# Optimization experiments

Hardware: AMD Instinct MI355X
Metric: run time of the kernel (lower is better)

The kernel has to match this reference:

```python
import jax, jax.numpy as jnp
import numpy as np

B = 4             # graphs per batch
POS_RANGE = 240.0 # pos lives in [0, 240)^3
VOXELS = (20.0, 30.0, 50.0, 80.0)
NEG = -1e30


def _basis(u):
    # open B-spline basis, degree 1, kernel_size 2, dim 3 -> 8 weights per edge
    cols = []
    for k in range(8):
        w = (u[:, 0] if k & 4 else 1.0 - u[:, 0])
        w = w * (u[:, 1] if k & 2 else 1.0 - u[:, 1])
        w = w * (u[:, 2] if k & 1 else 1.0 - u[:, 2])
        cols.append(w)
    return jnp.stack(cols, axis=1)  # [E, 8]


def _cartesian(pos, src, dst, emask):
    # T.Cartesian(cat=False, norm=True): rel pos scaled into [0,1]
    rel = pos[src] - pos[dst]
    m = jnp.max(jnp.where(emask[:, None], jnp.abs(rel), 0.0))
    return rel / (2.0 * jnp.maximum(m, 1e-9)) + 0.5


def _spline_conv(x, src, dst, pseudo, emask, W, Wr, b, n_nodes):
    # out_i = mean_{j->i} sum_k B_k(u_ij) x_j W_k + x_i Wr + b
    basis = _basis(pseudo) * emask[:, None].astype(x.dtype)  # [E,8]
    xk = jnp.einsum('ni,kio->nko', x, W)                     # [N,8,O]
    msg = basis[:, 0, None] * xk[src, 0]
    for k in range(1, 8):
        msg = msg + basis[:, k, None] * xk[src, k]           # [E,O]
    agg = jax.ops.segment_sum(msg, dst, num_segments=n_nodes)
    deg = jax.ops.segment_sum(emask.astype(x.dtype), dst, num_segments=n_nodes)
    return agg / jnp.maximum(deg, 1.0)[:, None] + x @ Wr + b


def _voxel_ids(pos, batch, vs):
    G = int(np.ceil(POS_RANGE / vs))
    c = jnp.clip(jnp.floor(pos / vs).astype(jnp.int64), 0, G - 1)
    cell = (c[:, 0] * G + c[:, 1]) * G + c[:, 2]
    return batch * (G ** 3) + cell, G ** 3


def _max_pool(x, pos, batch, valid, src, dst, emask, vs):
    # voxel-grid max pooling: nodes become fixed voxel cells (empty cells masked)
    nid, ncells = _voxel_ids(pos, batch, vs)
    n_new = B * ncells
    xm = jnp.where(valid[:, None], x, NEG)
    x_p = jax.ops.segment_max(xm, nid, num_segments=n_new)
    cnt = jax.ops.segment_sum(valid.astype(x.dtype), nid, num_segments=n_new)
    v_new = cnt > 0
    x_p = jnp.where(v_new[:, None], x_p, 0.0)
    pos_p = jax.ops.segment_sum(pos * valid[:, None].astype(pos.dtype), nid, num_segments=n_new)
    pos_p = pos_p / jnp.maximum(cnt, 1.0)[:, None]
    batch_p = jnp.arange(n_new, dtype=jnp.int64) // ncells
    # coarsen edges: remap to cells, drop self loops, coalesce at fixed size
    s2, d2 = nid[src], nid[dst]
    sent = n_new * n_new
    key = jnp.where(emask & (s2 != d2), s2 * n_new + d2, sent)
    uk = jnp.unique(key, size=key.shape[0], fill_value=sent)
    em = uk != sent
    uk = jnp.where(em, uk, 0)
    return x_p, pos_p, batch_p, v_new, uk // n_new, uk % n_new, em


def setup_inputs():
    key = jax.random.key(0)
    ks = jax.random.split(key, 24)
    NP, DEG = 5000, 8
    N = B * NP
    E = N * DEG
    x = jax.random.normal(ks[0], (N, 1), dtype=jnp.float32)
    pos = jax.random.uniform(ks[1], (N, 3), dtype=jnp.float32) * POS_RANGE
    src = jnp.repeat(jnp.arange(N, dtype=jnp.int64), DEG)
    delta = jax.random.randint(ks[2], (E,), 1, 100, dtype=jnp.int64)
    dst = (src // NP) * NP + (src % NP + delta) % NP   # intra-graph edges
    edge_index = jnp.stack([src, dst])
    batch = jnp.arange(N, dtype=jnp.int64) // NP
    sizes = [1, 64, 128, 256, 512]
    params = {}
    for l in range(4):
        ci, co = sizes[l], sizes[l + 1]
        params[f'W{l+1}'] = jax.random.normal(ks[3 + 3 * l], (8, ci, co), dtype=jnp.float32) / np.sqrt(8.0 * ci)
        params[f'Wr{l+1}'] = jax.random.normal(ks[4 + 3 * l], (ci, co), dtype=jnp.float32) / np.sqrt(float(ci))
        params[f'b{l+1}'] = jnp.zeros((co,), dtype=jnp.float32)
    params['fc1_w'] = jax.random.normal(ks[16], (64 * 512, 1024), dtype=jnp.float32) / np.sqrt(64.0 * 512.0)
    params['fc1_b'] = jnp.zeros((1024,), dtype=jnp.float32)
    params['fc2_w'] = jax.random.normal(ks[17], (1024, 1), dtype=jnp.float32) / np.sqrt(1024.0)
    params['fc2_b'] = jnp.zeros((1,), dtype=jnp.float32)
    return dict(x=x, pos=pos, edge_index=edge_index, batch=batch, **params)


def reference(x, pos, edge_index, batch, W1, Wr1, b1, W2, Wr2, b2, W3, Wr3, b3,
              W4, Wr4, b4, fc1_w, fc1_b, fc2_w, fc2_b):
    src, dst = edge_index[0], edge_index[1]
    n_nodes = x.shape[0]
    valid = jnp.ones((n_nodes,), dtype=bool)
    emask = jnp.ones((src.shape[0],), dtype=bool)
    Ws = [(W1, Wr1, b1), (W2, Wr2, b2), (W3, Wr3, b3), (W4, Wr4, b4)]
    for l in range(4):
        pseudo = _cartesian(pos, src, dst, emask)
        W, Wr, b = Ws[l]
        x = jax.nn.elu(_spline_conv(x, src, dst, pseudo, emask, W, Wr, b, n_nodes))
        if l < 3:
            x, pos, batch, valid, src, dst, emask = _max_pool(x, pos, batch, valid, src, dst, emask, VOXELS[l])
            n_nodes = x.shape[0]
    # MaxPoolingX(voxel=80, size=64): ceil(240/80)^3 = 27 <= 64 slots per graph
    nid, ncells = _voxel_ids(pos, batch, VOXELS[3])
    cluster = batch * 64 + (nid % ncells)
    xm = jnp.where(valid[:, None], x, NEG)
    xg = jax.ops.segment_max(xm, cluster, num_segments=B * 64)
    xg = jnp.where(xg <= NEG / 2, 0.0, xg)      # empty slots -> 0 (scatter-max default)
    xg = xg.reshape(B, 64 * 512)
    h = jax.nn.elu(xg @ fc1_w + fc1_b)           # dropout = identity (eval mode)
    return jax.nn.elu(h @ fc2_w + fc2_b)         # [B, 1]
```

## Files before the change

### kernel.cpp

```cpp
#include <hip/hip_runtime.h>

static constexpr int E0 = 160000;
static constexpr int NL0 = 20000;
static constexpr int NL1 = 6912;
static constexpr int NL2 = 2048;
static constexpr int NL3 = 500;

typedef short bf16x8 __attribute__((ext_vector_type(8)));
typedef float f32x4 __attribute__((ext_vector_type(4)));

__device__ __forceinline__ unsigned f2ord(float f) {
  unsigned u = __float_as_uint(f);
  return (u & 0x80000000u) ? ~u : (u | 0x80000000u);
}
__device__ __forceinline__ float ord2f(unsigned u) {
  unsigned v = (u & 0x80000000u) ? (u & 0x7fffffffu) : ~u;
  return __uint_as_float(v);
}
__device__ __forceinline__ float eluf(float x) { return x > 0.f ? x : expm1f(x); }
__device__ __forceinline__ void basis8(float u0, float u1, float u2, float* w) {
  float a0 = 1.f - u0, a1 = 1.f - u1, a2 = 1.f - u2;
  w[0] = a0*a1*a2; w[1] = a0*a1*u2; w[2] = a0*u1*a2; w[3] = a0*u1*u2;
  w[4] = u0*a1*a2; w[5] = u0*a1*u2; w[6] = u0*u1*a2; w[7] = u0*u1*u2;
}
__device__ __forceinline__ unsigned short f2b(float f) {
  unsigned u = __float_as_uint(f);
  return (unsigned short)((u + 0x7fffu + ((u >> 16) & 1u)) >> 16);
}
__device__ __forceinline__ float b2f(unsigned short h) {
  return __uint_as_float(((unsigned)h) << 16);
}
__device__ __forceinline__ int clampi(int v, int lo, int hi) {
  return v < lo ? lo : (v > hi ? hi : v);
}

__global__ void k_deg_absmax(const int* __restrict__ src, const int* __restrict__ dst,
                             const float* __restrict__ pos, int n,
                             int* __restrict__ degi, float* __restrict__ m) {
  float v = 0.f;
  for (int e = blockIdx.x * blockDim.x + threadIdx.x; e < n;
       e += gridDim.x * blockDim.x) {
    int s = src[e], d = dst[e];
    atomicAdd(&degi[d], 1);
    #pragma unroll
    for (int c = 0; c < 3; c++)
      v = fmaxf(v, fabsf(pos[s*3+c] - pos[d*3+c]));
  }
  for (int off = 32; off; off >>= 1) v = fmaxf(v, __shfl_down(v, off, 64));
  __shared__ float red[4];
  int lane = threadIdx.x & 63, wv = threadIdx.x >> 6;
  if (lane == 0) red[wv] = v;
  __syncthreads();
  if (threadIdx.x == 0) {
    float mm = fmaxf(fmaxf(red[0], red[1]), fmaxf(red[2], red[3]));
    atomicMax((unsigned*)m, __float_as_uint(mm));
  }
}

__global__ __launch_bounds__(256)
void k_wprep(const float* __restrict__ W1, const float* __restrict__ Wr1, float* __restrict__ wc1,
             const float* __restrict__ W2, const float* __restrict__ Wr2,
             const float* __restrict__ W3, const float* __restrict__ Wr3,
             const float* __restrict__ W4, const float* __restrict__ Wr4,
             unsigned short* __restrict__ w2h, unsigned short* __restrict__ w2l,
             unsigned short* __restrict__ w3h, unsigned short* __restrict__ w3l,
             unsigned short* __restrict__ w4h, unsigned short* __restrict__ w4l) {
  __shared__ float T[64][65];
  int b = blockIdx.x;
  const float *W, *Wr; unsigned short *oh, *ol; int K, N, kt, nt;
  if (b < 18)      { W = W2; Wr = Wr2; oh = w2h; ol = w2l; K = 576;  N = 128; kt = b / 2;        nt = b % 2; }
  else if (b < 90) { int q = b - 18; W = W3; Wr = Wr3; oh = w3h; ol = w3l; K = 1152; N = 256; kt = q / 4; nt = q % 4; }
  else             { int q = b - 90; W = W4; Wr = Wr4; oh = w4h; ol = w4l; K = 2304; N = 512; kt = q / 8; nt = q % 8; }
  int k0 = kt * 64, n0 = nt * 64, KW = K - K / 9;
  for (int i = threadIdx.x; i < 4096; i += 256) {
    int kk = i >> 6, nn = i & 63; int k = k0 + kk;
    T[kk][nn] = (k < KW) ? W[(long)k * N + n0 + nn] : Wr[(long)(k - KW) * N + n0 + nn];
  }
  __syncthreads();
  for (int i = threadIdx.x; i < 4096; i += 256) {
    int nn = i >> 6, kk = i & 63;
    float v = T[kk][nn];
    unsigned short hu = f2b(v);
    unsigned short lu = f2b(v - b2f(hu));
    long o = (long)(n0 + nn) * K + k0 + kk;
    oh[o] = hu; ol[o] = lu;
  }
  if (b == 0)
    for (int i = threadIdx.x; i < 576; i += 256)
      wc1[i] = (i < 512) ? W1[i] : Wr1[i - 512];
}

__global__ __launch_bounds__(1024)
void k_scan(int* __restrict__ degi, int* __restrict__ rowptr,
            int* __restrict__ cursor, int N) {
  __shared__ int wsum[16];
  __shared__ int woff[16];
  __shared__ int sbase, stot;
  int lane = threadIdx.x & 63, wv = threadIdx.x >> 6;
  if (threadIdx.x == 0) sbase = 0;
  __syncthreads();
  for (int c0 = 0; c0 < N; c0 += 1024) {
    int i = c0 + threadIdx.x;
    int v = (i < N) ? degi[i] : 0;
    int s = v;
    #pragma unroll
    for (int off = 1; off < 64; off <<= 1) {
      int t = __shfl_up(s, off, 64);
      if (lane >= off) s += t;
    }
    if (lane == 63) wsum[wv] = s;
    __syncthreads();
    if (threadIdx.x < 64) {
      int tv = (lane < 16) ? wsum[lane] : 0;
      int ss = tv;
      #pragma unroll
      for (int off = 1; off < 16; off <<= 1) {
        int t = __shfl_up(ss, off, 64);
        if (lane >= off) ss += t;
      }
      if (lane < 16) woff[lane] = ss - tv;
      if (lane == 15) stot = ss;
    }
    __syncthreads();
    int excl = sbase + woff[wv] + s - v;
    if (i < N) { rowptr[i] = excl; cursor[i] = excl; degi[i] = 0; }
    __syncthreads();
    if (threadIdx.x == 0) sbase += stot;
    __syncthreads();
  }
  if (threadIdx.x == 0) rowptr[N] = sbase;
}

__global__ void k_scatter(const int* __restrict__ src, const int* __restrict__ dst,
                          const int* __restrict__ ecnt, int ecap,
                          int* __restrict__ cursor, int* __restrict__ esrc,
                          unsigned* __restrict__ bm, long bmw) {
  long gs = (long)gridDim.x * blockDim.x;
  for (long i = (long)blockIdx.x * blockDim.x + threadIdx.x; i < bmw; i += gs) bm[i] = 0u;
  int n = ecnt ? *ecnt : ecap;
  for (int e = blockIdx.x * blockDim.x + threadIdx.x; e < n;
       e += gridDim.x * blockDim.x) {
    int p = atomicAdd(&cursor[dst[e]], 1);
    esrc[p] = src[e];
  }
}

__global__ __launch_bounds__(256)
void k_l1fused(const float* __restrict__ pos, const float* __restrict__ x0,
               const int* __restrict__ esrc, const int* __restrict__ rowptr,
               const float* __restrict__ m, const float* __restrict__ wc1,
               const float* __restrict__ b1,
               unsigned* __restrict__ pord, float* __restrict__ cnt,
               float* __restrict__ possum, int* __restrict__ nid) {
  int d = blockIdx.x * 4 + (threadIdx.x >> 6);
  int lane = threadIdx.x & 63;
  if (d >= NL0) return;
  float inv = 0.5f / fmaxf(m[0], 1e-9f);
  float pd0 = pos[d*3], pd1 = pos[d*3+1], pd2 = pos[d*3+2];
  int beg = rowptr[d], end = rowptr[d+1];
  float acc[8] = {};
  for (int j = beg; j < end; j++) {
    int s = esrc[j];
    float u0 = (pos[s*3+0] - pd0) * inv + 0.5f;
    float u1 = (pos[s*3+1] - pd1) * inv + 0.5f;
    float u2 = (pos[s*3+2] - pd2) * inv + 0.5f;
    float w[8]; basis8(u0, u1, u2, w);
    float xv = x0[s];
    #pragma unroll
    for (int k = 0; k < 8; k++) acc[k] += w[k] * xv;
  }
  float sc = 1.f / fmaxf((float)(end - beg), 1.f);
  float v = b1[lane] + x0[d] * wc1[512 + lane];
  #pragma unroll
  for (int k = 0; k < 8; k++) v += acc[k] * sc * wc1[k * 64 + lane];
  v = eluf(v);
  int c0 = clampi((int)floorf(pd0 / 20.f), 0, 11);
  int c1 = clampi((int)floorf(pd1 / 20.f), 0, 11);
  int c2 = clampi((int)floorf(pd2 / 20.f), 0, 11);
  int id = (d / 5000) * 1728 + (c0 * 12 + c1) * 12 + c2;
  atomicMax(&pord[(long)id * 64 + lane], f2ord(v));
  if (lane == 0) {
    nid[d] = id;
    atomicAdd(&cnt[id], 1.f);
    atomicAdd(&possum[id*3+0], pd0);
    atomicAdd(&possum[id*3+1], pd1);
    atomicAdd(&possum[id*3+2], pd2);
  }
}

__global__ __launch_bounds__(256)
void k_gather(const float* __restrict__ pos, const float* __restrict__ x,
              const int* __restrict__ esrc, const int* __restrict__ rowptr,
              const float* __restrict__ m,
              unsigned short* __restrict__ ysh, unsigned short* __restrict__ ysl,
              int N, int Ci, int nchunk,
              unsigned* __restrict__ zptr, long zn) {
  long gs = (long)gridDim.x * blockDim.x;
  for (long i = (long)blockIdx.x * blockDim.x + threadIdx.x; i < zn; i += gs) zptr[i] = 0u;
  int wid = blockIdx.x * 4 + (threadIdx.x >> 6);
  int lane = threadIdx.x & 63;
  int d = wid / nchunk, ch = wid % nchunk;
  if (d >= N) return;
  int co = ch * 64 + lane;
  float inv = 0.5f / fmaxf(m[0], 1e-9f);
  float pd0 = pos[d*3], pd1 = pos[d*3+1], pd2 = pos[d*3+2];
  int beg = rowptr[d], end = rowptr[d+1];
  float acc[8] = {};
  int s_cur = (beg < end) ? esrc[beg] : 0;
  for (int j = beg; j < end; j++) {
    int s = s_cur;
    s_cur = (j + 1 < end) ? esrc[j + 1] : 0;
    float u0 = (pos[s*3+0] - pd0) * inv + 0.5f;
    float u1 = (pos[s*3+1] - pd1) * inv + 0.5f;
    float u2 = (pos[s*3+2] - pd2) * inv + 0.5f;
    float w[8]; basis8(u0, u1, u2, w);
    float xv = x[(long)s * Ci + co];
    #pragma unroll
    for (int k = 0; k < 8; k++) acc[k] += w[k] * xv;
  }
  float sc = 1.f / fmaxf((float)(end - beg), 1.f);
  long row = (long)d * 9 * Ci;
  #pragma unroll
  for (int k = 0; k < 8; k++) {
    float v = acc[k] * sc;
    unsigned short hu = f2b(v);
    ysh[row + k * Ci + co] = hu;
    ysl[row + k * Ci + co] = f2b(v - b2f(hu));
  }
  float xd = x[(long)d * Ci + co];
  unsigned short hu = f2b(xd);
  ysh[row + 8 * Ci + co] = hu;
  ysl[row + 8 * Ci + co] = f2b(xd - b2f(hu));
}

__global__ __launch_bounds__(256)
void k_gemm_mfma(const unsigned short* __restrict__ Ah, const unsigned short* __restrict__ Al,
                 const unsigned short* __restrict__ Bh, const unsigned short* __restrict__ Bl,
                 float* __restrict__ Cp, int M, int N, int K, int ksl, long zstride) {
  __shared__ unsigned short Ash[64][40], Asl[64][40], Bsh[64][40], Bsl[64][40];
  int m0 = blockIdx.y * 64, n0 = blockIdx.x * 64;
  int kbeg = blockIdx.z * ksl;
  int t = threadIdx.x, w = t >> 6, lane = t & 63;
  int r = t >> 2, sg = (t & 3) * 8;
  f32x4 acc[4] = {};
  for (int kt = 0; kt < ksl; kt += 32) {
    bf16x8 va = {}, vb = {};
    if (m0 + r < M) {
      long ga = (long)(m0 + r) * K + kbeg + kt + sg;
      va = *(const bf16x8*)&Ah[ga];
      vb = *(const bf16x8*)&Al[ga];
    }
    *(bf16x8*)&Ash[r][sg] = va;
    *(bf16x8*)&Asl[r][sg] = vb;
    long gb = (long)(n0 + r) * K + kbeg + kt + sg;
    *(bf16x8*)&Bsh[r][sg] = *(const bf16x8*)&Bh[gb];
    *(bf16x8*)&Bsl[r][sg] = *(const bf16x8*)&Bl[gb];
    __syncthreads();
    int ar = (w << 4) + (lane & 15), kq = (lane >> 4) << 3;
    bf16x8 ah = *(const bf16x8*)&Ash[ar][kq];
    bf16x8 al = *(const bf16x8*)&Asl[ar][kq];
    #pragma unroll
    for (int nt = 0; nt < 4; nt++) {
      int br = (nt << 4) + (lane & 15);
      bf16x8 bh = *(const bf16x8*)&Bsh[br][kq];
      bf16x8 bl = *(const bf16x8*)&Bsl[br][kq];
      acc[nt] = __builtin_amdgcn_mfma_f32_16x16x32_bf16(al, bh, acc[nt], 0, 0, 0);
      acc[nt] = __builtin_amdgcn_mfma_f32_16x16x32_bf16(ah, bl, acc[nt], 0, 0, 0);
      acc[nt] = __builtin_amdgcn_mfma_f32_16x16x32_bf16(ah, bh, acc[nt], 0, 0, 0);
    }
    __syncthreads();
  }
  float* Co = Cp + zstride * blockIdx.z;
  int row0 = m0 + (w << 4) + ((lane >> 4) << 2);
  int col = n0 + (lane & 15);
  #pragma unroll
  for (int nt = 0; nt < 4; nt++)
    #pragma unroll
    for (int q = 0; q < 4; q++) {
      int gm = row0 + q;
      if (gm < M) Co[(long)gm * N + col + nt * 16] = acc[nt][q];
    }
}

__global__ void k_reduce_pool(const float* __restrict__ Cp, const float* __restrict__ bias,
                              long MN, int Co, int z,
                              const float* __restrict__ pos, const unsigned char* __restrict__ valid,
                              int div, float vs, int G, int SLOT,
                              unsigned* __restrict__ pord, float* __restrict__ cnt,
                              float* __restrict__ possum, int* __restrict__ nid) {
  long idx = (long)blockIdx.x * blockDim.x + threadIdx.x;
  if (idx >= MN) return;
  int n = (int)(idx / Co), o = (int)(idx % Co);
  float s = 0.f;
  for (int q = 0; q < z; q++) s += Cp[q * MN + idx];
  float v = eluf(s + bias[o]);
  float p0 = pos[n*3], p1 = pos[n*3+1], p2 = pos[n*3+2];
  int c0 = clampi((int)floorf(p0 / vs), 0, G - 1);
  int c1 = clampi((int)floorf(p1 / vs), 0, G - 1);
  int c2 = clampi((int)floorf(p2 / vs), 0, G - 1);
  int id = (n / div) * SLOT + (c0 * G + c1) * G + c2;
  if (o == 0 && nid) nid[n] = id;
  if (!valid[n]) return;
  atomicMax(&pord[(long)id * Co + o], f2ord(v));
  if (o == 0 && cnt) {
    atomicAdd(&cnt[id], 1.f);
    atomicAdd(&possum[id*3+0], p0);
    atomicAdd(&possum[id*3+1], p1);
    atomicAdd(&possum[id*3+2], p2);
  }
}

__global__ void k_pool_fin(const unsigned* __restrict__ pord, const float* __restrict__ cnt,
                           const float* __restrict__ possum, float* __restrict__ xp,
                           float* __restrict__ posp, unsigned char* __restrict__ validp,
                           int Nn, int Cf) {
  long idx = (long)blockIdx.x * blockDim.x + threadIdx.x;
  if (idx >= (long)Nn * Cf) return;
  int n = (int)(idx / Cf), o = (int)(idx % Cf);
  float c = cnt[n];
  xp[idx] = (c > 0.f) ? ord2f(pord[idx]) : 0.f;
  if (o == 0) {
    validp[n] = (c > 0.f) ? 1 : 0;
    float ic = 1.f / fmaxf(c, 1.f);
    posp[n*3+0] = possum[n*3+0] * ic;
    posp[n*3+1] = possum[n*3+1] * ic;
    posp[n*3+2] = possum[n*3+2] * ic;
  }
}

__global__ void k_pool_edges(const int* __restrict__ srcf, const int* __restrict__ dstf,
                             const int* __restrict__ ecntf, int ecap,
                             const int* __restrict__ nid, int Nn,
                             unsigned* __restrict__ bitmap,
                             int* __restrict__ srcc, int* __restrict__ dstc,
                             int* __restrict__ ecntc, int* __restrict__ degi,
                             const float* __restrict__ posp, float* __restrict__ m) {
  int n = ecntf ? *ecntf : ecap;
  float vmax = 0.f;
  for (int e = blockIdx.x * blockDim.x + threadIdx.x; e < n;
       e += gridDim.x * blockDim.x) {
    int s2 = nid[srcf[e]], d2 = nid[dstf[e]];
    if (s2 == d2) continue;
    #pragma unroll
    for (int c = 0; c < 3; c++)
      vmax = fmaxf(vmax, fabsf(posp[s2*3+c] - posp[d2*3+c]));
    unsigned key = (unsigned)s2 * (unsigned)Nn + (unsigned)d2;
    unsigned bit = 1u << (key & 31);
    unsigned old = atomicOr(&bitmap[key >> 5], bit);
    if (!(old & bit)) {
      int p = atomicAdd(ecntc, 1);
      srcc[p] = s2; dstc[p] = d2;
      atomicAdd(&degi[d2], 1);
    }
  }
  for (int off = 32; off; off >>= 1) vmax = fmaxf(vmax, __shfl_down(vmax, off, 64));
  __shared__ float red[4];
  int lane = threadIdx.x & 63, wv = threadIdx.x >> 6;
  if (lane == 0) red[wv] = vmax;
  __syncthreads();
  if (threadIdx.x == 0) {
    float mm = fmaxf(fmaxf(red[0], red[1]), fmaxf(red[2], red[3]));
    atomicMax((unsigned*)m, __float_as_uint(mm));
  }
}

__global__ __launch_bounds__(128)
void k_fc1(const unsigned* __restrict__ xg_ord, const float* __restrict__ w,
           float* __restrict__ h) {
  int cellhalf = blockIdx.x >> 3, jb = blockIdx.x & 7;
  int cell = cellhalf >> 1, half = cellhalf & 1;
  int j = jb * 128 + threadIdx.x;
  __shared__ float xs[4][256];
  for (int q = threadIdx.x; q < 1024; q += 128) {
    int b = q >> 8, ci = q & 255;
    unsigned o = xg_ord[((b * 64 + cell) << 9) + half * 256 + ci];
    xs[b][ci] = (o == 0u) ? 0.f : ord2f(o);
  }
  __syncthreads();
  float a0 = 0, a1 = 0, a2 = 0, a3 = 0;
  int cbase = cell * 512 + half * 256;
  for (int ci = 0; ci < 256; ci++) {
    float ww = w[(long)(cbase + ci) * 1024 + j];
    a0 += xs[0][ci] * ww; a1 += xs[1][ci] * ww;
    a2 += xs[2][ci] * ww; a3 += xs[3][ci] * ww;
  }
  atomicAdd(&h[j], a0);        atomicAdd(&h[1024 + j], a1);
  atomicAdd(&h[2048 + j], a2); atomicAdd(&h[3072 + j], a3);
}

__global__ void k_fc2(const float* __restrict__ h, const float* __restrict__ fb1,
                      const float* __restrict__ w, const float* __restrict__ b,
                      float* __restrict__ out) {
  int bb = blockIdx.x, t = threadIdx.x;
  float a = 0;
  for (int j = t; j < 1024; j += 256) a += eluf(h[bb * 1024 + j] + fb1[j]) * w[j];
  for (int off = 32; off; off >>= 1) a += __shfl_down(a, off, 64);
  __shared__ float red[4];
  int lane = t & 63, wv = t >> 6;
  if (lane == 0) red[wv] = a;
  __syncthreads();
  if (t == 0) out[bb] = eluf(red[0] + red[1] + red[2] + red[3] + b[0]);
}

extern "C" void kernel_launch(void* const* d_in, const int* in_sizes, int n_in,
                              void* d_out, int out_size, void* d_ws, size_t ws_size,
                              hipStream_t stream) {
  const float* x0   = (const float*)d_in[0];
  const float* pos0 = (const float*)d_in[1];
  const int*   ei   = (const int*)d_in[2];
  const float* W1 = (const float*)d_in[4],  *Wr1 = (const float*)d_in[5],  *b1 = (const float*)d_in[6];
  const float* W2 = (const float*)d_in[7],  *Wr2 = (const float*)d_in[8],  *b2 = (const float*)d_in[9];
  const float* W3 = (const float*)d_in[10], *Wr3 = (const float*)d_in[11], *b3 = (const float*)d_in[12];
  const float* W4 = (const float*)d_in[13], *Wr4 = (const float*)d_in[14], *b4 = (const float*)d_in[15];
  const float* fw1 = (const float*)d_in[16], *fb1 = (const float*)d_in[17];
  const float* fw2 = (const float*)d_in[18], *fb2 = (const float*)d_in[19];
  float* out = (float*)d_out;
  const int* src0 = ei;
  const int* dst0 = ei + E0;

  char* ws = (char*)d_ws;
  size_t off = 0;
  auto alloc = [&](size_t bytes) -> void* {
    off = (off + 255) & ~(size_t)255;
    void* p = ws + off; off += bytes; return p;
  };
  int* src1 = (int*)alloc(E0 * 4); int* dst1 = (int*)alloc(E0 * 4);
  int* src2 = (int*)alloc(E0 * 4); int* dst2 = (int*)alloc(E0 * 4);
  int* src3 = (int*)alloc(E0 * 4); int* dst3 = (int*)alloc(E0 * 4);
  float* x1p = (float*)alloc((size_t)NL1 * 64 * 4);
  float* x2p = (float*)alloc((size_t)NL2 * 128 * 4);
  float* x3p = (float*)alloc((size_t)NL3 * 256 * 4);
  float* pos1 = (float*)alloc(NL1 * 12);
  float* pos2 = (float*)alloc(NL2 * 12);
  float* pos3 = (float*)alloc(NL3 * 12);
  unsigned char* val1 = (unsigned char*)alloc(NL1);
  unsigned char* val2 = (unsigned char*)alloc(NL2);
  unsigned char* val3 = (unsigned char*)alloc(NL3);
  unsigned short* ysh = (unsigned short*)alloc((size_t)NL1 * 576 * 2);
  unsigned short* ysl = (unsigned short*)alloc((size_t)NL1 * 576 * 2);
  float* wc1 = (float*)alloc(576 * 4);
  unsigned short* w2h = (unsigned short*)alloc((size_t)576 * 128 * 2);
  unsigned short* w2l = (unsigned short*)alloc((size_t)576 * 128 * 2);
  unsigned short* w3h = (unsigned short*)alloc((size_t)1152 * 256 * 2);
  unsigned short* w3l = (unsigned short*)alloc((size_t)1152 * 256 * 2);
  unsigned short* w4h = (unsigned short*)alloc((size_t)2304 * 512 * 2);
  unsigned short* w4l = (unsigned short*)alloc((size_t)2304 * 512 * 2);
  float* Cp  = (float*)alloc((size_t)6 * 2048 * 256 * 4);
  int* nid    = (int*)alloc(NL0 * 4);
  int* rowptr = (int*)alloc((NL0 + 1) * 4);
  int* cursor = (int*)alloc(NL0 * 4);
  int* esrc   = (int*)alloc(E0 * 4);
  char* zA = (char*)alloc(0);
  float* h      = (float*)alloc(4096 * 4);
  float* cnt    = (float*)alloc(NL1 * 4);
  float* possum = (float*)alloc(NL1 * 12);
  unsigned* pord = (unsigned*)alloc((size_t)NL1 * 64 * 4);
  char* zAend = (char*)alloc(0);
  int* degi = (int*)alloc(NL0 * 4);
  size_t bmwords = ((size_t)NL1 * NL1 + 31) / 32;
  unsigned* bitmap = (unsigned*)alloc(bmwords * 4);
  float* mbuf = (float*)alloc(64);
  int* ecnt = (int*)(mbuf + 8);
  char* zend = (char*)alloc(0);
  long zAn = (long)(zAend - zA) / 4;
  size_t zbytes = (size_t)(zend - zA);
  unsigned* xg_ord = pord + (size_t)NL3 * 256;
  (void)ws_size; (void)in_sizes; (void)n_in; (void)out_size;

  auto cdiv = [](long a, long b) { return (int)((a + b - 1) / b); };

  hipMemsetAsync(zA, 0, zbytes, stream);

  k_deg_absmax<<<512, 256, 0, stream>>>(src0, dst0, pos0, E0, degi, mbuf + 0);
  k_wprep<<<378, 256, 0, stream>>>(W1, Wr1, wc1, W2, Wr2, W3, Wr3, W4, Wr4,
                                   w2h, w2l, w3h, w3l, w4h, w4l);
  k_scan<<<1, 1024, 0, stream>>>(degi, rowptr, cursor, NL0);
  k_scatter<<<512, 256, 0, stream>>>(src0, dst0, nullptr, E0, cursor, esrc, bitmap, bmwords);

  k_l1fused<<<5000, 256, 0, stream>>>(pos0, x0, esrc, rowptr, mbuf + 0, wc1, b1,
                                      pord, cnt, possum, nid);
  k_pool_fin<<<cdiv((long)NL1 * 64, 256), 256, 0, stream>>>(pord, cnt, possum, x1p, pos1, val1, NL1, 64);
  k_pool_edges<<<512, 256, 0, stream>>>(src0, dst0, nullptr, E0, nid, NL1, bitmap,
                                        src1, dst1, ecnt + 0, degi, pos1, mbuf + 1);
  k_scan<<<1, 1024, 0, stream>>>(degi, rowptr, cursor, NL1);
  k_scatter<<<512, 256, 0, stream>>>(src1, dst1, ecnt + 0, E0, cursor, esrc, bitmap, bmwords);

  k_gather<<<cdiv(NL1, 4), 256, 0, stream>>>(pos1, x1p, esrc, rowptr, mbuf + 1,
                                             ysh, ysl, NL1, 64, 1, (unsigned*)zA, zAn);
  k_gemm_mfma<<<dim3(2, cdiv(NL1, 64), 3), 256, 0, stream>>>(ysh, ysl, w2h, w2l, Cp,
                                                             NL1, 128, 576, 192, (long)NL1 * 128);
  k_reduce_pool<<<cdiv((long)NL1 * 128, 256), 256, 0, stream>>>(
      Cp, b2, (long)NL1 * 128, 128, 3, pos1, val1, 1728, 30.f, 8, 512, pord, cnt, possum, nid);
  k_pool_fin<<<cdiv((long)NL2 * 128, 256), 256, 0, stream>>>(pord, cnt, possum, x2p, pos2, val2, NL2, 128);
  k_pool_edges<<<512, 256, 0, stream>>>(src1, dst1, ecnt + 0, E0, nid, NL2, bitmap,
                                        src2, dst2, ecnt + 1, degi, pos2, mbuf + 2);
  k_scan<<<1, 1024, 0, stream>>>(degi, rowptr, cursor, NL2);
  k_scatter<<<512, 256, 0, stream>>>(src2, dst2, ecnt + 1, E0, cursor, esrc, bitmap, bmwords);

  k_gather<<<cdiv(NL2 * 2, 4), 256, 0, stream>>>(pos2, x2p, esrc, rowptr, mbuf + 2,
                                                 ysh, ysl, NL2, 128, 2, (unsigned*)zA, zAn);
  k_gemm_mfma<<<dim3(4, cdiv(NL2, 64), 6), 256, 0, stream>>>(ysh, ysl, w3h, w3l, Cp,
                                                             NL2, 256, 1152, 192, (long)NL2 * 256);
  k_reduce_pool<<<cdiv((long)NL2 * 256, 256), 256, 0, stream>>>(
      Cp, b3, (long)NL2 * 256, 256, 6, pos2, val2, 512, 50.f, 5, 125, pord, cnt, possum, nid);
  k_pool_fin<<<cdiv((long)NL3 * 256, 256), 256, 0, stream>>>(pord, cnt, possum, x3p, pos3, val3, NL3, 256);
  k_pool_edges<<<512, 256, 0, stream>>>(src2, dst2, ecnt + 1, E0, nid, NL3, bitmap,
                                        src3, dst3, ecnt + 2, degi, pos3, mbuf + 3);
  k_scan<<<1, 1024, 0, stream>>>(degi, rowptr, cursor, NL3);
  k_scatter<<<512, 256, 0, stream>>>(src3, dst3, ecnt + 2, E0, cursor, esrc, bitmap, bmwords);

  k_gather<<<cdiv(NL3 * 4, 4), 256, 0, stream>>>(pos3, x3p, esrc, rowptr, mbuf + 3,
                                                 ysh, ysl, NL3, 256, 4, (unsigned*)zA, zAn);
  k_gemm_mfma<<<dim3(8, cdiv(NL3, 64), 12), 256, 0, stream>>>(ysh, ysl, w4h, w4l, Cp,
                                                              NL3, 512, 2304, 192, (long)NL3 * 512);
  k_reduce_pool<<<cdiv((long)NL3 * 512, 256), 256, 0, stream>>>(
      Cp, b4, (long)NL3 * 512, 512, 12, pos3, val3, 125, 80.f, 3, 64, xg_ord, nullptr, nullptr, nullptr);

  k_fc1<<<27 * 2 * 8, 128, 0, stream>>>(xg_ord, fw1, h);
  k_fc2<<<4, 256, 0, stream>>>(h, fb1, fw2, fb2, out);
}
```

Baseline: 482.3 us.

## Replace CSR build with atomic linked lists and fuse GEMM with pooling

Replaces the degree-count, scan and scatter CSR construction with per-destination linked lists built through atomicExch. This removes the single-block scan kernels and several launches per layer. Pooling finalisation is folded into the consumers: gather reads pooled max, count and position sums directly, and the GEMM for layers 2 and 3 now runs without K-splitting and scatters pooled results itself. Separate per-layer buffers and bitmaps replace the shared ones. The trade-off is that linked-list traversal is a serially dependent pointer chase, and neighbour order is no longer deterministic.

```diff
diff --git a/kernel.cpp b/kernel.cpp
--- a/kernel.cpp
+++ b/kernel.cpp
@@ -34,229 +34,31 @@
   return v < lo ? lo : (v > hi ? hi : v);
 }
 
-__global__ void k_deg_absmax(const int* __restrict__ src, const int* __restrict__ dst,
-                             const float* __restrict__ pos, int n,
-                             int* __restrict__ degi, float* __restrict__ m) {
-  float v = 0.f;
-  for (int e = blockIdx.x * blockDim.x + threadIdx.x; e < n;
-       e += gridDim.x * blockDim.x) {
-    int s = src[e], d = dst[e];
-    atomicAdd(&degi[d], 1);
-    #pragma unroll
-    for (int c = 0; c < 3; c++)
-      v = fmaxf(v, fabsf(pos[s*3+c] - pos[d*3+c]));
-  }
-  for (int off = 32; off; off >>= 1) v = fmaxf(v, __shfl_down(v, off, 64));
-  __shared__ float red[4];
-  int lane = threadIdx.x & 63, wv = threadIdx.x >> 6;
-  if (lane == 0) red[wv] = v;
-  __syncthreads();
-  if (threadIdx.x == 0) {
-    float mm = fmaxf(fmaxf(red[0], red[1]), fmaxf(red[2], red[3]));
-    atomicMax((unsigned*)m, __float_as_uint(mm));
-  }
-}
-
-__global__ __launch_bounds__(256)
-void k_wprep(const float* __restrict__ W1, const float* __restrict__ Wr1, float* __restrict__ wc1,
-             const float* __restrict__ W2, const float* __restrict__ Wr2,
-             const float* __restrict__ W3, const float* __restrict__ Wr3,
-             const float* __restrict__ W4, const float* __restrict__ Wr4,
-             unsigned short* __restrict__ w2h, unsigned short* __restrict__ w2l,
-             unsigned short* __restrict__ w3h, unsigned short* __restrict__ w3l,
-             unsigned short* __restrict__ w4h, unsigned short* __restrict__ w4l) {
-  __shared__ float T[64][65];
-  int b = blockIdx.x;
-  const float *W, *Wr; unsigned short *oh, *ol; int K, N, kt, nt;
-  if (b < 18)      { W = W2; Wr = Wr2; oh = w2h; ol = w2l; K = 576;  N = 128; kt = b / 2;        nt = b % 2; }
-  else if (b < 90) { int q = b - 18; W = W3; Wr = Wr3; oh = w3h; ol = w3l; K = 1152; N = 256; kt = q / 4; nt = q % 4; }
-  else             { int q = b - 90; W = W4; Wr = Wr4; oh = w4h; ol = w4l; K = 2304; N = 512; kt = q / 8; nt = q % 8; }
-  int k0 = kt * 64, n0 = nt * 64, KW = K - K / 9;
-  for (int i = threadIdx.x; i < 4096; i += 256) {
-    int kk = i >> 6, nn = i & 63; int k = k0 + kk;
-    T[kk][nn] = (k < KW) ? W[(long)k * N + n0 + nn] : Wr[(long)(k - KW) * N + n0 + nn];
-  }
-  __syncthreads();
-  for (int i = threadIdx.x; i < 4096; i += 256) {
-    int nn = i >> 6, kk = i & 63;
-    float v = T[kk][nn];
-    unsigned short hu = f2b(v);
-    unsigned short lu = f2b(v - b2f(hu));
-    long o = (long)(n0 + nn) * K + k0 + kk;
-    oh[o] = hu; ol[o] = lu;
-  }
-  if (b == 0)
-    for (int i = threadIdx.x; i < 576; i += 256)
-      wc1[i] = (i < 512) ? W1[i] : Wr1[i - 512];
-}
-
-__global__ __launch_bounds__(1024)
-void k_scan(int* __restrict__ degi, int* __restrict__ rowptr,
-            int* __restrict__ cursor, int N) {
-  __shared__ int wsum[16];
-  __shared__ int woff[16];
-  __shared__ int sbase, stot;
-  int lane = threadIdx.x & 63, wv = threadIdx.x >> 6;
-  if (threadIdx.x == 0) sbase = 0;
-  __syncthreads();
-  for (int c0 = 0; c0 < N; c0 += 1024) {
-    int i = c0 + threadIdx.x;
-    int v = (i < N) ? degi[i] : 0;
-    int s = v;
-    #pragma unroll
-    for (int off = 1; off < 64; off <<= 1) {
-      int t = __shfl_up(s, off, 64);
-      if (lane >= off) s += t;
-    }
-    if (lane == 63) wsum[wv] = s;
-    __syncthreads();
-    if (threadIdx.x < 64) {
-      int tv = (lane < 16) ? wsum[lane] : 0;
-      int ss = tv;
-      #pragma unroll
-      for (int off = 1; off < 16; off <<= 1) {
-        int t = __shfl_up(ss, off, 64);
-        if (lane >= off) ss += t;
-      }
-      if (lane < 16) woff[lane] = ss - tv;
-      if (lane == 15) stot = ss;
-    }
-    __syncthreads();
-    int excl = sbase + woff[wv] + s - v;
-    if (i < N) { rowptr[i] = excl; cursor[i] = excl; degi[i] = 0; }
-    __syncthreads();
-    if (threadIdx.x == 0) sbase += stot;
-    __syncthreads();
-  }
-  if (threadIdx.x == 0) rowptr[N] = sbase;
-}
-
-__global__ void k_scatter(const int* __restrict__ src, const int* __restrict__ dst,
-                          const int* __restrict__ ecnt, int ecap,
-                          int* __restrict__ cursor, int* __restrict__ esrc,
-                          unsigned* __restrict__ bm, long bmw) {
-  long gs = (long)gridDim.x * blockDim.x;
-  for (long i = (long)blockIdx.x * blockDim.x + threadIdx.x; i < bmw; i += gs) bm[i] = 0u;
-  int n = ecnt ? *ecnt : ecap;
-  for (int e = blockIdx.x * blockDim.x + threadIdx.x; e < n;
-       e += gridDim.x * blockDim.x) {
-    int p = atomicAdd(&cursor[dst[e]], 1);
-    esrc[p] = src[e];
-  }
-}
-
-__global__ __launch_bounds__(256)
-void k_l1fused(const float* __restrict__ pos, const float* __restrict__ x0,
-               const int* __restrict__ esrc, const int* __restrict__ rowptr,
-               const float* __restrict__ m, const float* __restrict__ wc1,
-               const float* __restrict__ b1,
-               unsigned* __restrict__ pord, float* __restrict__ cnt,
-               float* __restrict__ possum, int* __restrict__ nid) {
-  int d = blockIdx.x * 4 + (threadIdx.x >> 6);
-  int lane = threadIdx.x & 63;
-  if (d >= NL0) return;
-  float inv = 0.5f / fmaxf(m[0], 1e-9f);
-  float pd0 = pos[d*3], pd1 = pos[d*3+1], pd2 = pos[d*3+2];
-  int beg = rowptr[d], end = rowptr[d+1];
-  float acc[8] = {};
-  for (int j = beg; j < end; j++) {
-    int s = esrc[j];
-    float u0 = (pos[s*3+0] - pd0) * inv + 0.5f;
-    float u1 = (pos[s*3+1] - pd1) * inv + 0.5f;
-    float u2 = (pos[s*3+2] - pd2) * inv + 0.5f;
-    float w[8]; basis8(u0, u1, u2, w);
-    float xv = x0[s];
-    #pragma unroll
-    for (int k = 0; k < 8; k++) acc[k] += w[k] * xv;
-  }
-  float sc = 1.f / fmaxf((float)(end - beg), 1.f);
-  float v = b1[lane] + x0[d] * wc1[512 + lane];
-  #pragma unroll
-  for (int k = 0; k < 8; k++) v += acc[k] * sc * wc1[k * 64 + lane];
-  v = eluf(v);
-  int c0 = clampi((int)floorf(pd0 / 20.f), 0, 11);
-  int c1 = clampi((int)floorf(pd1 / 20.f), 0, 11);
-  int c2 = clampi((int)floorf(pd2 / 20.f), 0, 11);
-  int id = (d / 5000) * 1728 + (c0 * 12 + c1) * 12 + c2;
-  atomicMax(&pord[(long)id * 64 + lane], f2ord(v));
-  if (lane == 0) {
-    nid[d] = id;
-    atomicAdd(&cnt[id], 1.f);
-    atomicAdd(&possum[id*3+0], pd0);
-    atomicAdd(&possum[id*3+1], pd1);
-    atomicAdd(&possum[id*3+2], pd2);
-  }
-}
-
-__global__ __launch_bounds__(256)
-void k_gather(const float* __restrict__ pos, const float* __restrict__ x,
-              const int* __restrict__ esrc, const int* __restrict__ rowptr,
-              const float* __restrict__ m,
-              unsigned short* __restrict__ ysh, unsigned short* __restrict__ ysl,
-              int N, int Ci, int nchunk,
-              unsigned* __restrict__ zptr, long zn) {
-  long gs = (long)gridDim.x * blockDim.x;
-  for (long i = (long)blockIdx.x * blockDim.x + threadIdx.x; i < zn; i += gs) zptr[i] = 0u;
-  int wid = blockIdx.x * 4 + (threadIdx.x >> 6);
-  int lane = threadIdx.x & 63;
-  int d = wid / nchunk, ch = wid % nchunk;
-  if (d >= N) return;
-  int co = ch * 64 + lane;
-  float inv = 0.5f / fmaxf(m[0], 1e-9f);
-  float pd0 = pos[d*3], pd1 = pos[d*3+1], pd2 = pos[d*3+2];
-  int beg = rowptr[d], end = rowptr[d+1];
-  float acc[8] = {};
-  int s_cur = (beg < end) ? esrc[beg] : 0;
-  for (int j = beg; j < end; j++) {
-    int s = s_cur;
-    s_cur = (j + 1 < end) ? esrc[j + 1] : 0;
-    float u0 = (pos[s*3+0] - pd0) * inv + 0.5f;
-    float u1 = (pos[s*3+1] - pd1) * inv + 0.5f;
-    float u2 = (pos[s*3+2] - pd2) * inv + 0.5f;
-    float w[8]; basis8(u0, u1, u2, w);
-    float xv = x[(long)s * Ci + co];
-    #pragma unroll
-    for (int k = 0; k < 8; k++) acc[k] += w[k] * xv;
-  }
-  float sc = 1.f / fmaxf((float)(end - beg), 1.f);
-  long row = (long)d * 9 * Ci;
-  #pragma unroll
-  for (int k = 0; k < 8; k++) {
-    float v = acc[k] * sc;
-    unsigned short hu = f2b(v);
-    ysh[row + k * Ci + co] = hu;
-    ysl[row + k * Ci + co] = f2b(v - b2f(hu));
-  }
-  float xd = x[(long)d * Ci + co];
-  unsigned short hu = f2b(xd);
-  ysh[row + 8 * Ci + co] = hu;
-  ysl[row + 8 * Ci + co] = f2b(xd - b2f(hu));
-}
-
-__global__ __launch_bounds__(256)
-void k_gemm_mfma(const unsigned short* __restrict__ Ah, const unsigned short* __restrict__ Al,
-                 const unsigned short* __restrict__ Bh, const unsigned short* __restrict__ Bl,
-                 float* __restrict__ Cp, int M, int N, int K, int ksl, long zstride) {
-  __shared__ unsigned short Ash[64][40], Asl[64][40], Bsh[64][40], Bsl[64][40];
-  int m0 = blockIdx.y * 64, n0 = blockIdx.x * 64;
-  int kbeg = blockIdx.z * ksl;
-  int t = threadIdx.x, w = t >> 6, lane = t & 63;
+__device__ __forceinline__ void mfma_tile(const unsigned short* __restrict__ Ah,
+    const unsigned short* __restrict__ Al, const unsigned short* __restrict__ Bh,
+    const unsigned short* __restrict__ Bl, int M, long K, int m0, int n0,
+    int kbeg, int ksl, char* smem, f32x4* acc) {
+  auto Ash = (unsigned short (*)[40])(smem);
+  auto Asl = (unsigned short (*)[40])(smem + 5120);
+  auto Bsh = (unsigned short (*)[40])(smem + 10240);
+  auto Bsl = (unsigned short (*)[40])(smem + 15360);
+  int t = threadIdx.x;
   int r = t >> 2, sg = (t & 3) * 8;
-  f32x4 acc[4] = {};
+  int w = t >> 6, lane = t & 63;
+  int ar = (w << 4) + (lane & 15), kq = (lane >> 4) << 3;
   for (int kt = 0; kt < ksl; kt += 32) {
-    bf16x8 va = {}, vb = {};
+    bf16x8 va = {}, vl = {};
     if (m0 + r < M) {
       long ga = (long)(m0 + r) * K + kbeg + kt + sg;
       va = *(const bf16x8*)&Ah[ga];
-      vb = *(const bf16x8*)&Al[ga];
+      vl = *(const bf16x8*)&Al[ga];
     }
     *(bf16x8*)&Ash[r][sg] = va;
-    *(bf16x8*)&Asl[r][sg] = vb;
+    *(bf16x8*)&Asl[r][sg] = vl;
     long gb = (long)(n0 + r) * K + kbeg + kt + sg;
     *(bf16x8*)&Bsh[r][sg] = *(const bf16x8*)&Bh[gb];
     *(bf16x8*)&Bsl[r][sg] = *(const bf16x8*)&Bl[gb];
     __syncthreads();
-    int ar = (w << 4) + (lane & 15), kq = (lane >> 4) << 3;
     bf16x8 ah = *(const bf16x8*)&Ash[ar][kq];
     bf16x8 al = *(const bf16x8*)&Asl[ar][kq];
     #pragma unroll
@@ -270,98 +72,276 @@
     }
     __syncthreads();
   }
-  float* Co = Cp + zstride * blockIdx.z;
+}
+
+__global__ __launch_bounds__(256)
+void k_prep(const int* __restrict__ src0, const int* __restrict__ dst0,
+            const float* __restrict__ pos0, int* __restrict__ head0,
+            int* __restrict__ next0, float* __restrict__ mbuf,
+            const float* __restrict__ W1, const float* __restrict__ Wr1, float* __restrict__ wc1,
+            const float* __restrict__ W2, const float* __restrict__ Wr2,
+            const float* __restrict__ W3, const float* __restrict__ Wr3,
+            const float* __restrict__ W4, const float* __restrict__ Wr4,
+            unsigned short* __restrict__ w2h, unsigned short* __restrict__ w2l,
+            unsigned short* __restrict__ w3h, unsigned short* __restrict__ w3l,
+            unsigned short* __restrict__ w4h, unsigned short* __restrict__ w4l) {
+  __shared__ __align__(16) float T[64][65];
+  __shared__ float red[4];
+  int tid = blockIdx.x * 256 + threadIdx.x, gsz = gridDim.x * 256;
+  float v = 0.f;
+  for (int e = tid; e < E0; e += gsz) {
+    int s = src0[e], d = dst0[e];
+    next0[e] = atomicExch(&head0[d], e + 1);
+    v = fmaxf(v, fabsf(pos0[s*3]   - pos0[d*3]));
+    v = fmaxf(v, fabsf(pos0[s*3+1] - pos0[d*3+1]));
+    v = fmaxf(v, fabsf(pos0[s*3+2] - pos0[d*3+2]));
+  }
+  #pragma unroll
+  for (int off = 32; off; off >>= 1) v = fmaxf(v, __shfl_down(v, off, 64));
+  if ((threadIdx.x & 63) == 0) red[threadIdx.x >> 6] = v;
+  __syncthreads();
+  if (threadIdx.x == 0)
+    atomicMax((unsigned*)mbuf,
+              __float_as_uint(fmaxf(fmaxf(red[0], red[1]), fmaxf(red[2], red[3]))));
+  for (int b = blockIdx.x; b < 378; b += gridDim.x) {
+    const float *W, *Wr; unsigned short *oh, *ol; int K, N, kt, nt;
+    if (b < 18)      { W = W2; Wr = Wr2; oh = w2h; ol = w2l; K = 576;  N = 128; kt = b / 2; nt = b % 2; }
+    else if (b < 90) { int q = b - 18; W = W3; Wr = Wr3; oh = w3h; ol = w3l; K = 1152; N = 256; kt = q / 4; nt = q % 4; }
+    else             { int q = b - 90; W = W4; Wr = Wr4; oh = w4h; ol = w4l; K = 2304; N = 512; kt = q / 8; nt = q % 8; }
+    int k0 = kt * 64, n0 = nt * 64, KW = K - K / 9;
+    __syncthreads();
+    for (int i = threadIdx.x; i < 4096; i += 256) {
+      int kk = i >> 6, nn = i & 63, k = k0 + kk;
+      T[kk][nn] = (k < KW) ? W[(long)k * N + n0 + nn] : Wr[(long)(k - KW) * N + n0 + nn];
+    }
+    __syncthreads();
+    for (int i = threadIdx.x; i < 4096; i += 256) {
+      int nn = i >> 6, kk = i & 63;
+      float vv = T[kk][nn];
+      unsigned short hu = f2b(vv), lu = f2b(vv - b2f(hu));
+      long o = (long)(n0 + nn) * K + k0 + kk;
+      oh[o] = hu; ol[o] = lu;
+    }
+  }
+  if (blockIdx.x == 0)
+    for (int i = threadIdx.x; i < 576; i += 256)
+      wc1[i] = (i < 512) ? W1[i] : Wr1[i - 512];
+}
+
+__global__ __launch_bounds__(256)
+void k_l1(const float* __restrict__ pos0, const float* __restrict__ x0,
+          const int* __restrict__ src0, const int* __restrict__ head0,
+          const int* __restrict__ next0, const float* __restrict__ mbuf,
+          const float* __restrict__ wc1, const float* __restrict__ b1,
+          unsigned* __restrict__ pord1, float* __restrict__ cnt1,
+          float* __restrict__ possum1, int* __restrict__ nid) {
+  int d = blockIdx.x * 4 + (threadIdx.x >> 6);
+  int lane = threadIdx.x & 63;
+  if (d >= NL0) return;
+  float inv = 0.5f / fmaxf(mbuf[0], 1e-9f);
+  float pd0 = pos0[d*3], pd1 = pos0[d*3+1], pd2 = pos0[d*3+2];
+  float acc[8] = {};
+  int len = 0;
+  for (int j = head0[d]; j; ) {
+    int e = j - 1; j = next0[e];
+    int s = src0[e];
+    float u0 = (pos0[s*3]   - pd0) * inv + 0.5f;
+    float u1 = (pos0[s*3+1] - pd1) * inv + 0.5f;
+    float u2 = (pos0[s*3+2] - pd2) * inv + 0.5f;
+    float w[8]; basis8(u0, u1, u2, w);
+    float xv = x0[s];
+    #pragma unroll
+    for (int k = 0; k < 8; k++) acc[k] += w[k] * xv;
+    len++;
+  }
+  float sc = 1.f / fmaxf((float)len, 1.f);
+  float v = b1[lane] + x0[d] * wc1[512 + lane];
+  #pragma unroll
+  for (int k = 0; k < 8; k++) v += acc[k] * sc * wc1[k * 64 + lane];
+  v = eluf(v);
+  int c0 = clampi((int)floorf(pd0 / 20.f), 0, 11);
+  int c1 = clampi((int)floorf(pd1 / 20.f), 0, 11);
+  int c2 = clampi((int)floorf(pd2 / 20.f), 0, 11);
+  int id = (d / 5000) * 1728 + (c0 * 12 + c1) * 12 + c2;
+  atomicMax(&pord1[(long)id * 64 + lane], f2ord(v));
+  if (lane == 0) {
+    nid[d] = id;
+    atomicAdd(&cnt1[id], 1.f);
+    atomicAdd(&possum1[id*3],   pd0);
+    atomicAdd(&possum1[id*3+1], pd1);
+    atomicAdd(&possum1[id*3+2], pd2);
+  }
+}
+
+__global__ __launch_bounds__(256)
+void k_pedge(const int* __restrict__ srcf, const int* __restrict__ dstf,
+             const int* __restrict__ ecntf, int ecap,
+             const int* __restrict__ nid, int Nn, unsigned* __restrict__ bitmap,
+             int* __restrict__ srcc, int* __restrict__ dstc, int* __restrict__ nextc,
+             int* __restrict__ headc, int* __restrict__ ecntc,
+             const float* __restrict__ possum, const float* __restrict__ cnt,
+             float* __restrict__ mo) {
+  __shared__ float red[4];
+  int n = ecntf ? *ecntf : ecap;
+  float vmax = 0.f;
+  for (int e = blockIdx.x * 256 + threadIdx.x; e < n; e += gridDim.x * 256) {
+    int s2 = nid[srcf[e]], d2 = nid[dstf[e]];
+    if (s2 == d2) continue;
+    float ics = 1.f / fmaxf(cnt[s2], 1.f), icd = 1.f / fmaxf(cnt[d2], 1.f);
+    vmax = fmaxf(vmax, fabsf(possum[s2*3]   * ics - possum[d2*3]   * icd));
+    vmax = fmaxf(vmax, fabsf(possum[s2*3+1] * ics - possum[d2*3+1] * icd));
+    vmax = fmaxf(vmax, fabsf(possum[s2*3+2] * ics - possum[d2*3+2] * icd));
+    unsigned key = (unsigned)s2 * (unsigned)Nn + (unsigned)d2;
+    unsigned bit = 1u << (key & 31);
+    unsigned old = atomicOr(&bitmap[key >> 5], bit);
+    if (!(old & bit)) {
+      int q = atomicAdd(ecntc, 1);
+      srcc[q] = s2; dstc[q] = d2;
+      nextc[q] = atomicExch(&headc[d2], q + 1);
+    }
+  }
+  #pragma unroll
+  for (int off = 32; off; off >>= 1) vmax = fmaxf(vmax, __shfl_down(vmax, off, 64));
+  if ((threadIdx.x & 63) == 0) red[threadIdx.x >> 6] = vmax;
+  __syncthreads();
+  if (threadIdx.x == 0)
+    atomicMax((unsigned*)mo,
+              __float_as_uint(fmaxf(fmaxf(red[0], red[1]), fmaxf(red[2], red[3]))));
+}
+
+__global__ __launch_bounds__(256)
+void k_gather(const float* __restrict__ possum, const float* __restrict__ cnt,
+              const unsigned* __restrict__ pordc,
+              const int* __restrict__ srcarr, const int* __restrict__ head,
+              const int* __restrict__ nextl, const float* __restrict__ mbuf,
+              unsigned short* __restrict__ ysh, unsigned short* __restrict__ ysl,
+              int N, int Ci, int nchunk) {
+  int wid = blockIdx.x * 4 + (threadIdx.x >> 6);
+  int lane = threadIdx.x & 63;
+  int d = wid / nchunk, ch = wid % nchunk;
+  if (d >= N) return;
+  int co = ch * 64 + lane;
+  float inv = 0.5f / fmaxf(mbuf[0], 1e-9f);
+  float cd = cnt[d];
+  float icd = 1.f / fmaxf(cd, 1.f);
+  float pd0 = possum[d*3] * icd, pd1 = possum[d*3+1] * icd, pd2 = possum[d*3+2] * icd;
+  float acc[8] = {};
+  int len = 0;
+  for (int j = head[d]; j; ) {
+    int e = j - 1; j = nextl[e];
+    int s = srcarr[e];
+    float ics = 1.f / fmaxf(cnt[s], 1.f);
+    float u0 = (possum[s*3]   * ics - pd0) * inv + 0.5f;
+    float u1 = (possum[s*3+1] * ics - pd1) * inv + 0.5f;
+    float u2 = (possum[s*3+2] * ics - pd2) * inv + 0.5f;
+    float w[8]; basis8(u0, u1, u2, w);
+    float xv = ord2f(pordc[(long)s * Ci + co]);
+    #pragma unroll
+    for (int k = 0; k < 8; k++) acc[k] += w[k] * xv;
+    len++;
+  }
+  float sc = 1.f / fmaxf((float)len, 1.f);
+  long row = (long)d * 9 * Ci;
+  #pragma unroll
+  for (int k = 0; k < 8; k++) {
+    float v = acc[k] * sc;
+    unsigned short hu = f2b(v);
+    ysh[row + k * Ci + co] = hu;
+    ysl[row + k * Ci + co] = f2b(v - b2f(hu));
+  }
+  float xd = (cd > 0.f) ? ord2f(pordc[(long)d * Ci + co]) : 0.f;
+  unsigned short hu = f2b(xd);
+  ysh[row + 8 * Ci + co] = hu;
+  ysl[row + 8 * Ci + co] = f2b(xd - b2f(hu));
+}
+
+__global__ __launch_bounds__(256)
+void k_gemmpool(const unsigned short* __restrict__ ysh, const unsigned short* __restrict__ ysl,
+                const unsigned short* __restrict__ Bh, const unsigned short* __restrict__ Bl,
+                int M, int N, int K, const float* __restrict__ bias,
+                const float* __restrict__ possum, const float* __restrict__ cnt,
+                int div, float vs, int G, int NC,
+                unsigned* __restrict__ pordn, float* __restrict__ cntn,
+                float* __restrict__ possumn, int* __restrict__ nid) {
+  __shared__ __align__(16) char smem[20480];
+  int nbx = N >> 6;
+  int bx = blockIdx.x % nbx, by = blockIdx.x / nbx;
+  int m0 = by * 64, n0 = bx * 64;
+  f32x4 acc[4] = {};
+  mfma_tile(ysh, ysl, Bh, Bl, M, K, m0, n0, 0, K, smem, acc);
+  int w = threadIdx.x >> 6, lane = threadIdx.x & 63;
   int row0 = m0 + (w << 4) + ((lane >> 4) << 2);
-  int col = n0 + (lane & 15);
+  int colb = n0 + (lane & 15);
+  #pragma unroll
+  for (int q = 0; q < 4; q++) {
+    int gm = row0 + q;
+    float c = cnt[gm];
+    float ic = 1.f / fmaxf(c, 1.f);
+    float p0 = possum[gm*3] * ic, p1 = possum[gm*3+1] * ic, p2 = possum[gm*3+2] * ic;
+    int c0 = clampi((int)floorf(p0 / vs), 0, G - 1);
+    int c1 = clampi((int)floorf(p1 / vs), 0, G - 1);
+    int c2 = clampi((int)floorf(p2 / vs), 0, G - 1);
+    int id = (gm / div) * NC + (c0 * G + c1) * G + c2;
+    bool vl = c > 0.f;
+    if (bx == 0 && (lane & 15) == 0) {
+      nid[gm] = id;
+      if (vl) {
+        atomicAdd(&cntn[id], 1.f);
+        atomicAdd(&possumn[id*3],   p0);
+        atomicAdd(&possumn[id*3+1], p1);
+        atomicAdd(&possumn[id*3+2], p2);
+      }
+    }
+    if (vl) {
+      #pragma unroll
+      for (int nt = 0; nt < 4; nt++) {
+        int col = colb + nt * 16;
+        float v = eluf(acc[nt][q] + bias[col]);
+        atomicMax(&pordn[(long)id * N + col], f2ord(v));
+      }
+    }
+  }
+}
+
+__global__ __launch_bounds__(256)
+void k_gemm4(const unsigned short* __restrict__ ysh, const unsigned short* __restrict__ ysl,
+             const unsigned short* __restrict__ Bh, const unsigned short* __restrict__ Bl,
+             float* __restrict__ Cp) {
+  __shared__ __align__(16) char smem[20480];
+  int z = blockIdx.x >> 6, rem = blockIdx.x & 63, bx = rem & 7, by = rem >> 3;
+  int m0 = by * 64, n0 = bx * 64;
+  f32x4 acc[4] = {};
+  mfma_tile(ysh, ysl, Bh, Bl, 500, 2304, m0, n0, z * 576, 576, smem, acc);
+  float* Co = Cp + (long)z * 256000;
+  int w = threadIdx.x >> 6, lane = threadIdx.x & 63;
+  int row0 = m0 + (w << 4) + ((lane >> 4) << 2);
+  int colb = n0 + (lane & 15);
   #pragma unroll
   for (int nt = 0; nt < 4; nt++)
     #pragma unroll
     for (int q = 0; q < 4; q++) {
       int gm = row0 + q;
-      if (gm < M) Co[(long)gm * N + col + nt * 16] = acc[nt][q];
-    }
-}
-
-__global__ void k_reduce_pool(const float* __restrict__ Cp, const float* __restrict__ bias,
-                              long MN, int Co, int z,
-                              const float* __restrict__ pos, const unsigned char* __restrict__ valid,
-                              int div, float vs, int G, int SLOT,
-                              unsigned* __restrict__ pord, float* __restrict__ cnt,
-                              float* __restrict__ possum, int* __restrict__ nid) {
-  long idx = (long)blockIdx.x * blockDim.x + threadIdx.x;
-  if (idx >= MN) return;
-  int n = (int)(idx / Co), o = (int)(idx % Co);
-  float s = 0.f;
-  for (int q = 0; q < z; q++) s += Cp[q * MN + idx];
-  float v = eluf(s + bias[o]);
-  float p0 = pos[n*3], p1 = pos[n*3+1], p2 = pos[n*3+2];
-  int c0 = clampi((int)floorf(p0 / vs), 0, G - 1);
-  int c1 = clampi((int)floorf(p1 / vs), 0, G - 1);
-  int c2 = clampi((int)floorf(p2 / vs), 0, G - 1);
-  int id = (n / div) * SLOT + (c0 * G + c1) * G + c2;
-  if (o == 0 && nid) nid[n] = id;
-  if (!valid[n]) return;
-  atomicMax(&pord[(long)id * Co + o], f2ord(v));
-  if (o == 0 && cnt) {
-    atomicAdd(&cnt[id], 1.f);
-    atomicAdd(&possum[id*3+0], p0);
-    atomicAdd(&possum[id*3+1], p1);
-    atomicAdd(&possum[id*3+2], p2);
-  }
-}
-
-__global__ void k_pool_fin(const unsigned* __restrict__ pord, const float* __restrict__ cnt,
-                           const float* __restrict__ possum, float* __restrict__ xp,
-                           float* __restrict__ posp, unsigned char* __restrict__ validp,
-                           int Nn, int Cf) {
-  long idx = (long)blockIdx.x * blockDim.x + threadIdx.x;
-  if (idx >= (long)Nn * Cf) return;
-  int n = (int)(idx / Cf), o = (int)(idx % Cf);
-  float c = cnt[n];
-  xp[idx] = (c > 0.f) ? ord2f(pord[idx]) : 0.f;
-  if (o == 0) {
-    validp[n] = (c > 0.f) ? 1 : 0;
-    float ic = 1.f / fmaxf(c, 1.f);
-    posp[n*3+0] = possum[n*3+0] * ic;
-    posp[n*3+1] = possum[n*3+1] * ic;
-    posp[n*3+2] = possum[n*3+2] * ic;
-  }
-}
-
-__global__ void k_pool_edges(const int* __restrict__ srcf, const int* __restrict__ dstf,
-                             const int* __restrict__ ecntf, int ecap,
-                             const int* __restrict__ nid, int Nn,
-                             unsigned* __restrict__ bitmap,
-                             int* __restrict__ srcc, int* __restrict__ dstc,
-                             int* __restrict__ ecntc, int* __restrict__ degi,
-                             const float* __restrict__ posp, float* __restrict__ m) {
-  int n = ecntf ? *ecntf : ecap;
-  float vmax = 0.f;
-  for (int e = blockIdx.x * blockDim.x + threadIdx.x; e < n;
-       e += gridDim.x * blockDim.x) {
-    int s2 = nid[srcf[e]], d2 = nid[dstf[e]];
-    if (s2 == d2) continue;
-    #pragma unroll
-    for (int c = 0; c < 3; c++)
-      vmax = fmaxf(vmax, fabsf(posp[s2*3+c] - posp[d2*3+c]));
-    unsigned key = (unsigned)s2 * (unsigned)Nn + (unsigned)d2;
-    unsigned bit = 1u << (key & 31);
-    unsigned old = atomicOr(&bitmap[key >> 5], bit);
-    if (!(old & bit)) {
-      int p = atomicAdd(ecntc, 1);
-      srcc[p] = s2; dstc[p] = d2;
-      atomicAdd(&degi[d2], 1);
-    }
-  }
-  for (int off = 32; off; off >>= 1) vmax = fmaxf(vmax, __shfl_down(vmax, off, 64));
-  __shared__ float red[4];
-  int lane = threadIdx.x & 63, wv = threadIdx.x >> 6;
-  if (lane == 0) red[wv] = vmax;
-  __syncthreads();
-  if (threadIdx.x == 0) {
-    float mm = fmaxf(fmaxf(red[0], red[1]), fmaxf(red[2], red[3]));
-    atomicMax((unsigned*)m, __float_as_uint(mm));
-  }
+      if (gm < 500) Co[(long)gm * 512 + colb + nt * 16] = acc[nt][q];
+    }
+}
+
+__global__ void k_reduce4(const float* __restrict__ Cp, const float* __restrict__ b4,
+                          const float* __restrict__ possum3, const float* __restrict__ cnt3,
+                          unsigned* __restrict__ xg) {
+  int idx = blockIdx.x * 256 + threadIdx.x;
+  if (idx >= 256000) return;
+  int n = idx >> 9, o = idx & 511;
+  float s = Cp[idx] + Cp[idx + 256000] + Cp[idx + 512000] + Cp[idx + 768000];
+  float v = eluf(s + b4[o]);
+  float c = cnt3[n];
+  if (c <= 0.f) return;
+  float ic = 1.f / c;
+  float p0 = possum3[n*3] * ic, p1 = possum3[n*3+1] * ic, p2 = possum3[n*3+2] * ic;
+  int c0 = clampi((int)floorf(p0 / 80.f), 0, 2);
+  int c1 = clampi((int)floorf(p1 / 80.f), 0, 2);
+  int c2 = clampi((int)floorf(p2 / 80.f), 0, 2);
+  int cl = (n / 125) * 64 + (c0 * 3 + c1) * 3 + c2;
+  atomicMax(&xg[(long)cl * 512 + o], f2ord(v));
 }
 
 __global__ __launch_bounds__(128)
@@ -422,20 +402,13 @@
   size_t off = 0;
   auto alloc = [&](size_t bytes) -> void* {
     off = (off + 255) & ~(size_t)255;
-    void* p = ws + off; off += bytes; return p;
+    void* q = ws + off; off += bytes; return q;
   };
-  int* src1 = (int*)alloc(E0 * 4); int* dst1 = (int*)alloc(E0 * 4);
-  int* src2 = (int*)alloc(E0 * 4); int* dst2 = (int*)alloc(E0 * 4);
-  int* src3 = (int*)alloc(E0 * 4); int* dst3 = (int*)alloc(E0 * 4);
-  float* x1p = (float*)alloc((size_t)NL1 * 64 * 4);
-  float* x2p = (float*)alloc((size_t)NL2 * 128 * 4);
-  float* x3p = (float*)alloc((size_t)NL3 * 256 * 4);
-  float* pos1 = (float*)alloc(NL1 * 12);
-  float* pos2 = (float*)alloc(NL2 * 12);
-  float* pos3 = (float*)alloc(NL3 * 12);
-  unsigned char* val1 = (unsigned char*)alloc(NL1);
-  unsigned char* val2 = (unsigned char*)alloc(NL2);
-  unsigned char* val3 = (unsigned char*)alloc(NL3);
+  int* next0 = (int*)alloc(E0 * 4);
+  int* src1 = (int*)alloc(E0 * 4); int* dst1 = (int*)alloc(E0 * 4); int* next1 = (int*)alloc(E0 * 4);
+  int* src2 = (int*)alloc(E0 * 4); int* dst2 = (int*)alloc(E0 * 4); int* next2 = (int*)alloc(E0 * 4);
+  int* src3 = (int*)alloc(E0 * 4); int* dst3 = (int*)alloc(E0 * 4); int* next3 = (int*)alloc(E0 * 4);
+  int* nid  = (int*)alloc(NL0 * 4);
   unsigned short* ysh = (unsigned short*)alloc((size_t)NL1 * 576 * 2);
   unsigned short* ysl = (unsigned short*)alloc((size_t)NL1 * 576 * 2);
   float* wc1 = (float*)alloc(576 * 4);
@@ -445,77 +418,67 @@
   unsigned short* w3l = (unsigned short*)alloc((size_t)1152 * 256 * 2);
   unsigned short* w4h = (unsigned short*)alloc((size_t)2304 * 512 * 2);
   unsigned short* w4l = (unsigned short*)alloc((size_t)2304 * 512 * 2);
-  float* Cp  = (float*)alloc((size_t)6 * 2048 * 256 * 4);
-  int* nid    = (int*)alloc(NL0 * 4);
-  int* rowptr = (int*)alloc((NL0 + 1) * 4);
-  int* cursor = (int*)alloc(NL0 * 4);
-  int* esrc   = (int*)alloc(E0 * 4);
-  char* zA = (char*)alloc(0);
-  float* h      = (float*)alloc(4096 * 4);
-  float* cnt    = (float*)alloc(NL1 * 4);
-  float* possum = (float*)alloc(NL1 * 12);
-  unsigned* pord = (unsigned*)alloc((size_t)NL1 * 64 * 4);
-  char* zAend = (char*)alloc(0);
-  int* degi = (int*)alloc(NL0 * 4);
-  size_t bmwords = ((size_t)NL1 * NL1 + 31) / 32;
-  unsigned* bitmap = (unsigned*)alloc(bmwords * 4);
+  float* Cp = (float*)alloc((size_t)4 * 256000 * 4);
+  char* z0 = (char*)alloc(0);
+  int* head0 = (int*)alloc(NL0 * 4);
+  int* head1 = (int*)alloc(NL1 * 4);
+  int* head2 = (int*)alloc(NL2 * 4);
+  int* head3 = (int*)alloc(NL3 * 4);
+  unsigned* pord1 = (unsigned*)alloc((size_t)NL1 * 64 * 4);
+  unsigned* pord2 = (unsigned*)alloc((size_t)NL2 * 128 * 4);
+  unsigned* pord3 = (unsigned*)alloc((size_t)NL3 * 256 * 4);
+  unsigned* xg    = (unsigned*)alloc((size_t)4 * 64 * 512 * 4);
+  float* cnt1 = (float*)alloc(NL1 * 4);
+  float* cnt2 = (float*)alloc(NL2 * 4);
+  float* cnt3 = (float*)alloc(NL3 * 4);
+  float* possum1 = (float*)alloc(NL1 * 12);
+  float* possum2 = (float*)alloc(NL2 * 12);
+  float* possum3 = (float*)alloc(NL3 * 12);
+  size_t bm1w = ((size_t)NL1 * NL1 + 31) / 32;
+  size_t bm2w = ((size_t)NL2 * NL2 + 31) / 32;
+  size_t bm3w = ((size_t)NL3 * NL3 + 31) / 32;
+  unsigned* bm1 = (unsigned*)alloc(bm1w * 4);
+  unsigned* bm2 = (unsigned*)alloc(bm2w * 4);
+  unsigned* bm3 = (unsigned*)alloc(bm3w * 4);
   float* mbuf = (float*)alloc(64);
   int* ecnt = (int*)(mbuf + 8);
+  float* h = (float*)alloc(4096 * 4);
   char* zend = (char*)alloc(0);
-  long zAn = (long)(zAend - zA) / 4;
-  size_t zbytes = (size_t)(zend - zA);
-  unsigned* xg_ord = pord + (size_t)NL3 * 256;
+  size_t zbytes = (size_t)(zend - z0);
   (void)ws_size; (void)in_sizes; (void)n_in; (void)out_size;
 
   auto cdiv = [](long a, long b) { return (int)((a + b - 1) / b); };
 
-  hipMemsetAsync(zA, 0, zbytes, stream);
-
-  k_deg_absmax<<<512, 256, 0, stream>>>(src0, dst0, pos0, E0, degi, mbuf + 0);
-  k_wprep<<<378, 256, 0, stream>>>(W1, Wr1, wc1, W2, Wr2, W3, Wr3, W4, Wr4,
-                                   w2h, w2l, w3h, w3l, w4h, w4l);
-  k_scan<<<1, 1024, 0, stream>>>(degi, rowptr, cursor, NL0);
-  k_scatter<<<512, 256, 0, stream>>>(src0, dst0, nullptr, E0, cursor, esrc, bitmap, bmwords);
-
-  k_l1fused<<<5000, 256, 0, stream>>>(pos0, x0, esrc, rowptr, mbuf + 0, wc1, b1,
-                                      pord, cnt, possum, nid);
-  k_pool_fin<<<cdiv((long)NL1 * 64, 256), 256, 0, stream>>>(pord, cnt, possum, x1p, pos1, val1, NL1, 64);
-  k_pool_edges<<<512, 256, 0, stream>>>(src0, dst0, nullptr, E0, nid, NL1, bitmap,
-                                        src1, dst1, ecnt + 0, degi, pos1, mbuf + 1);
-  k_scan<<<1, 1024, 0, stream>>>(degi, rowptr, cursor, NL1);
-  k_scatter<<<512, 256, 0, stream>>>(src1, dst1, ecnt + 0, E0, cursor, esrc, bitmap, bmwords);
-
-  k_gather<<<cdiv(NL1, 4), 256, 0, stream>>>(pos1, x1p, esrc, rowptr, mbuf + 1,
-                                             ysh, ysl, NL1, 64, 1, (unsigned*)zA, zAn);
-  k_gemm_mfma<<<dim3(2, cdiv(NL1, 64), 3), 256, 0, stream>>>(ysh, ysl, w2h, w2l, Cp,
-                                                             NL1, 128, 576, 192, (long)NL1 * 128);
-  k_reduce_pool<<<cdiv((long)NL1 * 128, 256), 256, 0, stream>>>(
-      Cp, b2, (long)NL1 * 128, 128, 3, pos1, val1, 1728, 30.f, 8, 512, pord, cnt, possum, nid);
-  k_pool_fin<<<cdiv((long)NL2 * 128, 256), 256, 0, stream>>>(pord, cnt, possum, x2p, pos2, val2, NL2, 128);
-  k_pool_edges<<<512, 256, 0, stream>>>(src1, dst1, ecnt + 0, E0, nid, NL2, bitmap,
-                                        src2, dst2, ecnt + 1, degi, pos2, mbuf + 2);
-  k_scan<<<1, 1024, 0, stream>>>(degi, rowptr, cursor, NL2);
-  k_scatter<<<512, 256, 0, stream>>>(src2, dst2, ecnt + 1, E0, cursor, esrc, bitmap, bmwords);
-
-  k_gather<<<cdiv(NL2 * 2, 4), 256, 0, stream>>>(pos2, x2p, esrc, rowptr, mbuf + 2,
-                                                 ysh, ysl, NL2, 128, 2, (unsigned*)zA, zAn);
-  k_gemm_mfma<<<dim3(4, cdiv(NL2, 64), 6), 256, 0, stream>>>(ysh, ysl, w3h, w3l, Cp,
-                                                             NL2, 256, 1152, 192, (long)NL2 * 256);
-  k_reduce_pool<<<cdiv((long)NL2 * 256, 256), 256, 0, stream>>>(
-      Cp, b3, (long)NL2 * 256, 256, 6, pos2, val2, 512, 50.f, 5, 125, pord, cnt, possum, nid);
-  k_pool_fin<<<cdiv((long)NL3 * 256, 256), 256, 0, stream>>>(pord, cnt, possum, x3p, pos3, val3, NL3, 256);
-  k_pool_edges<<<512, 256, 0, stream>>>(src2, dst2, ecnt + 1, E0, nid, NL3, bitmap,
-                                        src3, dst3, ecnt + 2, degi, pos3, mbuf + 3);
-  k_scan<<<1, 1024, 0, stream>>>(degi, rowptr, cursor, NL3);
-  k_scatter<<<512, 256, 0, stream>>>(src3, dst3, ecnt + 2, E0, cursor, esrc, bitmap, bmwords);
-
-  k_gather<<<cdiv(NL3 * 4, 4), 256, 0, stream>>>(pos3, x3p, esrc, rowptr, mbuf + 3,
-                                                 ysh, ysl, NL3, 256, 4, (unsigned*)zA, zAn);
-  k_gemm_mfma<<<dim3(8, cdiv(NL3, 64), 12), 256, 0, stream>>>(ysh, ysl, w4h, w4l, Cp,
-                                                              NL3, 512, 2304, 192, (long)NL3 * 512);
-  k_reduce_pool<<<cdiv((long)NL3 * 512, 256), 256, 0, stream>>>(
-      Cp, b4, (long)NL3 * 512, 512, 12, pos3, val3, 125, 80.f, 3, 64, xg_ord, nullptr, nullptr, nullptr);
-
-  k_fc1<<<27 * 2 * 8, 128, 0, stream>>>(xg_ord, fw1, h);
+  hipMemsetAsync(z0, 0, zbytes, stream);
+
+  k_prep<<<512, 256, 0, stream>>>(src0, dst0, pos0, head0, next0, mbuf,
+                                  W1, Wr1, wc1, W2, Wr2, W3, Wr3, W4, Wr4,
+                                  w2h, w2l, w3h, w3l, w4h, w4l);
+  k_l1<<<cdiv(NL0, 4), 256, 0, stream>>>(pos0, x0, src0, head0, next0, mbuf,
+                                         wc1, b1, pord1, cnt1, possum1, nid);
+  k_pedge<<<512, 256, 0, stream>>>(src0, dst0, nullptr, E0, nid, NL1, bm1,
+                                   src1, dst1, next1, head1, ecnt + 0,
+                                   possum1, cnt1, mbuf + 1);
+  k_gather<<<cdiv(NL1, 4), 256, 0, stream>>>(possum1, cnt1, pord1, src1, head1, next1,
+                                             mbuf + 1, ysh, ysl, NL1, 64, 1);
+  k_gemmpool<<<(128 / 64) * (NL1 / 64), 256, 0, stream>>>(
+      ysh, ysl, w2h, w2l, NL1, 128, 576, b2, possum1, cnt1,
+      1728, 30.f, 8, 512, pord2, cnt2, possum2, nid);
+  k_pedge<<<512, 256, 0, stream>>>(src1, dst1, ecnt + 0, E0, nid, NL2, bm2,
+                                   src2, dst2, next2, head2, ecnt + 1,
+                                   possum2, cnt2, mbuf + 2);
+  k_gather<<<cdiv(NL2 * 2, 4), 256, 0, stream>>>(possum2, cnt2, pord2, src2, head2, next2,
+                                                 mbuf + 2, ysh, ysl, NL2, 128, 2);
+  k_gemmpool<<<(256 / 64) * (NL2 / 64), 256, 0, stream>>>(
+      ysh, ysl, w3h, w3l, NL2, 256, 1152, b3, possum2, cnt2,
+      512, 50.f, 5, 125, pord3, cnt3, possum3, nid);
+  k_pedge<<<512, 256, 0, stream>>>(src2, dst2, ecnt + 1, E0, nid, NL3, bm3,
+                                   src3, dst3, next3, head3, ecnt + 2,
+                                   possum3, cnt3, mbuf + 3);
+  k_gather<<<cdiv(NL3 * 4, 4), 256, 0, stream>>>(possum3, cnt3, pord3, src3, head3, next3,
+                                                 mbuf + 3, ysh, ysl, NL3, 256, 4);
+  k_gemm4<<<256, 256, 0, stream>>>(ysh, ysl, w4h, w4l, Cp);
+  k_reduce4<<<cdiv(256000, 256), 256, 0, stream>>>(Cp, b4, possum3, cnt3, xg);
+  k_fc1<<<27 * 2 * 8, 128, 0, stream>>>(xg, fw1, h);
   k_fc2<<<4, 256, 0, stream>>>(h, fb1, fw2, fb2, out);
 }
```

After: 427.6 us. 11.3% less time.
